# Optimization experiments

Hardware: AMD Instinct MI355X
Metric: run time of the kernel (lower is better)

The kernel has to match this reference:

```python
import jax, jax.numpy as jnp
import numpy as np

N, D, H, E = 4096, 256, 8, 131072
HD = D // H
EPS = 1e-5


def layernorm(x, g, b):
    mu = jnp.mean(x, axis=-1, keepdims=True)
    var = jnp.mean((x - mu) ** 2, axis=-1, keepdims=True)
    return (x - mu) * jax.lax.rsqrt(var + EPS) * g + b


def setup_inputs() -> dict:
    key = jax.random.key(0)
    ks = jax.random.split(key, 20)
    s = 1.0 / np.sqrt(D)
    x = jax.random.normal(ks[0], (N, D), jnp.float32)
    adj = jax.random.uniform(ks[1], (N, N)) < 0.01
    adj_mask = adj | jnp.eye(N, dtype=bool)  # self-loops keep softmax rows finite
    edge_index = jax.random.randint(ks[2], (2, E), 0, N, dtype=jnp.int64)
    edge_attr = jax.random.normal(ks[3], (E, D), jnp.float32)
    p = {
        'wq': jax.random.normal(ks[4], (D, D)) * s, 'bq': jnp.zeros((D,)),
        'wk': jax.random.normal(ks[5], (D, D)) * s, 'bk': jnp.zeros((D,)),
        'wv': jax.random.normal(ks[6], (D, D)) * s, 'bv': jnp.zeros((D,)),
        'wo': jax.random.normal(ks[7], (D, D)) * s, 'bo': jnp.zeros((D,)),
        'we': jax.random.normal(ks[8], (D, H)) * s, 'be': jnp.zeros((H,)),
        'w1': jax.random.normal(ks[9], (D, 4 * D)) * s, 'b1': jnp.zeros((4 * D,)),
        'w2': jax.random.normal(ks[10], (4 * D, D)) * (1.0 / np.sqrt(4 * D)), 'b2': jnp.zeros((D,)),
        'g1': jnp.ones((D,)), 'beta1': jnp.zeros((D,)),
        'g2': jnp.ones((D,)), 'beta2': jnp.zeros((D,)),
    }
    return dict(x=x, adj_mask=adj_mask, edge_index=edge_index, edge_attr=edge_attr, **p)


def reference(x, adj_mask, edge_index, edge_attr, wq, bq, wk, bk, wv, bv, wo, bo,
              we, be, w1, b1, w2, b2, g1, beta1, g2, beta2):
    n = x.shape[0]
    Q = (x @ wq + bq).reshape(n, H, HD)
    K = (x @ wk + bk).reshape(n, H, HD)
    V = (x @ wv + bv).reshape(n, H, HD)
    scores = jnp.einsum('nhd,mhd->nmh', Q, K) / np.sqrt(HD)  # [N,N,H]
    edge_bias = edge_attr @ we + be                          # [E,H]
    scores = scores.at[edge_index[0], edge_index[1]].add(edge_bias)
    s = jnp.transpose(scores, (0, 2, 1))                     # [N,H,N]
    s = jnp.where(adj_mask[:, None, :], s, -jnp.inf)
    attn = jax.nn.softmax(s, axis=-1)                        # dropout eval-mode no-op
    ctx = jnp.einsum('nhm,mhd->nhd', attn, V).reshape(n, D)
    attn_out = ctx @ wo + bo
    x1 = layernorm(x + attn_out, g1, beta1)
    ff = jax.nn.gelu(x1 @ w1 + b1, approximate=False) @ w2 + b2
    return layernorm(x1 + ff, g2, beta2)
```

## Files before the change

kernel.cpp:

```cpp
#include <hip/hip_runtime.h>
#include <math.h>

#define NN   4096
#define DD   256
#define HH   8
#define HD   32
#define DFF  1024
#define QKVW 768
#define AC   128
#define EC   128
#define SCPAD 129
#define QSP  36
#define NPB  2

typedef unsigned short ushort_t;
typedef __attribute__((ext_vector_type(8))) short short8;
typedef __attribute__((ext_vector_type(4))) float f32x4;

__device__ __forceinline__ float bf2f(unsigned short u){
  union { unsigned int i; float f; } v; v.i = ((unsigned int)u) << 16; return v.f;
}
__device__ __forceinline__ unsigned short f2bf(float f){
  union { float f; unsigned int i; } v; v.f = f;
  unsigned int x = v.i;
  return (unsigned short)((x + 0x7FFFu + ((x >> 16) & 1u)) >> 16);
}
__device__ __forceinline__ float ldf(const void* p, size_t i, int isbf){
  return isbf ? bf2f(((const ushort_t*)p)[i]) : ((const float*)p)[i];
}
__device__ __forceinline__ ushort_t ldb16(const void* p, size_t i, int isbf){
  return isbf ? ((const ushort_t*)p)[i] : f2bf(((const float*)p)[i]);
}

__global__ void k_detect(const int* __restrict__ adj32, const int* __restrict__ ei32,
                         const unsigned int* __restrict__ g1w, int* __restrict__ flags,
                         int* __restrict__ counts, int* __restrict__ cursor){
  __shared__ int c0s, c1s;
  int t = threadIdx.x;
  if (t == 0) { c0s = 0; c1s = 0; }
  __syncthreads();
  int c0 = 0, c1 = 0;
  for (int i = t; i < 960; i += 256) if (adj32[(size_t)i * 4097] != 0) c0++;
  for (int i = t; i < 2048; i += 256) if (ei32[2*i + 1] != 0) c1++;
  atomicAdd(&c0s, c0); atomicAdd(&c1s, c1);
  for (int i = t; i < NN; i += 256) { counts[i] = 0; cursor[i] = 0; }
  __syncthreads();
  if (t == 0) {
    flags[0] = (c0s == 960) ? 1 : 0;
    flags[1] = (c1s > 100) ? 1 : 0;
    flags[2] = (g1w[0] == 0x3F803F80u) ? 1 : 0;
  }
}

__global__ __launch_bounds__(256) void k_csr(const void* __restrict__ adj,
                                             const int* __restrict__ flags,
                                             int* __restrict__ alist,
                                             int* __restrict__ acnt){
  __shared__ int cntS;
  __shared__ int actS[AC];
  const int n = blockIdx.x, t = threadIdx.x;
  if (t == 0) cntS = 0;
  __syncthreads();
  if (flags[0]) {
    const uint4* arow = (const uint4*)((const int*)adj + (size_t)n * NN);
    #pragma unroll
    for (int i = 0; i < 4; i++) {
      uint4 v = arow[t + 256 * i];
      int c0 = 4 * (t + 256 * i);
      if (v.x) { int p = atomicAdd(&cntS, 1); if (p < AC) actS[p] = c0; }
      if (v.y) { int p = atomicAdd(&cntS, 1); if (p < AC) actS[p] = c0 + 1; }
      if (v.z) { int p = atomicAdd(&cntS, 1); if (p < AC) actS[p] = c0 + 2; }
      if (v.w) { int p = atomicAdd(&cntS, 1); if (p < AC) actS[p] = c0 + 3; }
    }
  } else {
    const uint4* arow = (const uint4*)((const unsigned char*)adj + (size_t)n * NN);
    uint4 v = arow[t];
    unsigned int wsv[4] = {v.x, v.y, v.z, v.w};
    #pragma unroll
    for (int q = 0; q < 4; q++) {
      unsigned int u = wsv[q];
      int c0 = 16 * t + 4 * q;
      if (u & 0x000000FFu) { int p = atomicAdd(&cntS, 1); if (p < AC) actS[p] = c0; }
      if (u & 0x0000FF00u) { int p = atomicAdd(&cntS, 1); if (p < AC) actS[p] = c0 + 1; }
      if (u & 0x00FF0000u) { int p = atomicAdd(&cntS, 1); if (p < AC) actS[p] = c0 + 2; }
      if (u & 0xFF000000u) { int p = atomicAdd(&cntS, 1); if (p < AC) actS[p] = c0 + 3; }
    }
  }
  __syncthreads();
  int m = cntS; if (m > AC) m = AC;
  if (t == 0) acnt[n] = m;
  for (int j = t; j < m; j += 256) alist[(size_t)n * AC + j] = actS[j];
}

#define NX    (NN * DD)
#define NWE   (DD * HH)
#define TPREP 768
__global__ __launch_bounds__(256) void k_prep(
    const void* __restrict__ x, const void* __restrict__ wq, const void* __restrict__ wk,
    const void* __restrict__ wv, const void* __restrict__ wo, const void* __restrict__ w1,
    const void* __restrict__ w2, const void* __restrict__ we,
    const void* __restrict__ bq, const void* __restrict__ bk, const void* __restrict__ bv,
    const void* __restrict__ bo, const void* __restrict__ be, const void* __restrict__ b1,
    const void* __restrict__ b2, const void* __restrict__ g1, const void* __restrict__ be1,
    const void* __restrict__ g2, const void* __restrict__ be2,
    const int* __restrict__ ei, const int* __restrict__ flags,
    ushort_t* __restrict__ xb,
    ushort_t* __restrict__ wqkvT, ushort_t* __restrict__ woT,
    ushort_t* __restrict__ w1T, ushort_t* __restrict__ w2T,
    float* __restrict__ wef, float* __restrict__ bqkvf,
    float* __restrict__ bof, float* __restrict__ bef,
    float* __restrict__ b1f, float* __restrict__ b2f,
    float* __restrict__ g1f, float* __restrict__ be1f,
    float* __restrict__ g2f, float* __restrict__ be2f,
    int* __restrict__ counts, int E, int TOT)
{
  const int isbf = flags[2];
  const int t = threadIdx.x;
  if (blockIdx.x < TPREP) {
    __shared__ ushort_t tile[32][36];
    int b = blockIdx.x;
    const void* src; ushort_t* dst; int R, C, ti;
    if (b < 64)       { src = wq; dst = wqkvT;              R = 256;  C = 256;  ti = b; }
    else if (b < 128) { src = wk; dst = wqkvT + 256 * 256;  R = 256;  C = 256;  ti = b - 64; }
    else if (b < 192) { src = wv; dst = wqkvT + 512 * 256;  R = 256;  C = 256;  ti = b - 128; }
    else if (b < 256) { src = wo; dst = woT;                R = 256;  C = 256;  ti = b - 192; }
    else if (b < 512) { src = w1; dst = w1T;                R = 256;  C = 1024; ti = b - 256; }
    else              { src = w2; dst = w2T;                R = 1024; C = 256;  ti = b - 512; }
    int tiles_c = C >> 5;
    int tr = ti / tiles_c, tc = ti - tr * tiles_c;
    int lr = t >> 3, lc0 = (t & 7) << 2;
    size_t sbase = (size_t)(tr * 32 + lr) * C + tc * 32 + lc0;
    if (isbf) {
      const ushort_t* s16 = (const ushort_t*)src + sbase;
      tile[lr][lc0+0] = s16[0]; tile[lr][lc0+1] = s16[1];
      tile[lr][lc0+2] = s16[2]; tile[lr][lc0+3] = s16[3];
    } else {
      const float4* sf = (const float4*)((const float*)src + sbase);
      float4 v = *sf;
      tile[lr][lc0+0] = f2bf(v.x); tile[lr][lc0+1] = f2bf(v.y);
      tile[lr][lc0+2] = f2bf(v.z); tile[lr][lc0+3] = f2bf(v.w);
    }
    __syncthreads();
    int i = t >> 3, j0 = (t & 7) << 2;
    ushort_t* dp = dst + (size_t)(tc * 32 + i) * R + tr * 32 + j0;
    ushort_t o0 = tile[j0][i], o1 = tile[j0+1][i], o2 = tile[j0+2][i], o3 = tile[j0+3][i];
    dp[0] = o0; dp[1] = o1; dp[2] = o2; dp[3] = o3;
    return;
  }
  const int ei32 = flags[1];
  const int stride = (gridDim.x - TPREP) * 256;
  for (int i = (blockIdx.x - TPREP) * 256 + t; i < TOT; i += stride) {
    int r = i;
    if (r < NX) { xb[r] = ldb16(x, r, isbf); continue; }
    r -= NX;
    if (r < E) {
      int src = ei32 ? ei[r] : ei[2 * r];
      if ((unsigned)src < (unsigned)NN) atomicAdd(&counts[src], 1);
      continue;
    }
    r -= E;
    if (r < NWE) { wef[r] = ldf(we, r, isbf); continue; }
    r -= NWE;
    if (r < QKVW) {
      const void* bs = (r < 256) ? bq : (r < 512) ? bk : bv;
      bqkvf[r] = ldf(bs, r & 255, isbf);
      continue;
    }
    r -= QKVW;
    if (r < DD)  { bof[r] = ldf(bo, r, isbf); continue; }   r -= DD;
    if (r < HH)  { bef[r] = ldf(be, r, isbf); continue; }   r -= HH;
    if (r < DFF) { b1f[r] = ldf(b1, r, isbf); continue; }   r -= DFF;
    if (r < DD)  { b2f[r] = ldf(b2, r, isbf); continue; }   r -= DD;
    if (r < DD)  { g1f[r] = ldf(g1, r, isbf); continue; }   r -= DD;
    if (r < DD)  { be1f[r] = ldf(be1, r, isbf); continue; } r -= DD;
    if (r < DD)  { g2f[r] = ldf(g2, r, isbf); continue; }   r -= DD;
    if (r < DD)  { be2f[r] = ldf(be2, r, isbf); }
  }
}

#define LDK 72
__global__ __launch_bounds__(256) void k_gemm(
    const ushort_t* __restrict__ A, const ushort_t* __restrict__ Bt,
    const float* __restrict__ bias, void* __restrict__ C,
    int M, int Nn, int K, int act, int mode,
    float* __restrict__ qf, ushort_t* __restrict__ kbuf, ushort_t* __restrict__ vbuf)
{
  __shared__ ushort_t As[64 * LDK];
  __shared__ ushort_t Bs[64 * LDK];
  const int t = threadIdx.x;
  const int wave = t >> 6, lane = t & 63;
  const int l15 = lane & 15, quad = lane >> 4;
  const int wr = wave >> 1, wc = wave & 1;
  const int bm0 = blockIdx.y * 64, bn0 = blockIdx.x * 64;

  const int arow = t >> 2, akg = (t & 3) << 4;

  f32x4 acc[2][2] = {};

  const ushort_t* ap = A  + (size_t)(bm0 + arow) * K + akg;
  const ushort_t* bp = Bt + (size_t)(bn0 + arow) * K + akg;
  uint4 a0 = *(const uint4*)ap;
  uint4 a1 = *(const uint4*)(ap + 8);
  uint4 b0 = *(const uint4*)bp;
  uint4 b1 = *(const uint4*)(bp + 8);

  for (int k0 = 0; k0 < K; k0 += 64) {
    __syncthreads();
    *(uint4*)(&As[arow * LDK + akg]) = a0;
    *(uint4*)(&As[arow * LDK + akg + 8]) = a1;
    *(uint4*)(&Bs[arow * LDK + akg]) = b0;
    *(uint4*)(&Bs[arow * LDK + akg + 8]) = b1;
    __syncthreads();
    if (k0 + 64 < K) {
      a0 = *(const uint4*)(ap + k0 + 64);
      a1 = *(const uint4*)(ap + k0 + 64 + 8);
      b0 = *(const uint4*)(bp + k0 + 64);
      b1 = *(const uint4*)(bp + k0 + 64 + 8);
    }
    #pragma unroll
    for (int kk = 0; kk < 2; kk++) {
      short8 af[2], bf[2];
      #pragma unroll
      for (int fr = 0; fr < 2; fr++)
        af[fr] = *(const short8*)(&As[(wr * 32 + fr * 16 + l15) * LDK + kk * 32 + quad * 8]);
      #pragma unroll
      for (int fc = 0; fc < 2; fc++)
        bf[fc] = *(const short8*)(&Bs[(wc * 32 + fc * 16 + l15) * LDK + kk * 32 + quad * 8]);
      #pragma unroll
      for (int fr = 0; fr < 2; fr++)
        #pragma unroll
        for (int fc = 0; fc < 2; fc++)
          acc[fr][fc] = __builtin_amdgcn_mfma_f32_16x16x32_bf16(af[fr], bf[fc], acc[fr][fc], 0, 0, 0);
    }
  }

  #pragma unroll
  for (int fr = 0; fr < 2; fr++) {
    #pragma unroll
    for (int fc = 0; fc < 2; fc++) {
      int gn = bn0 + wc * 32 + fc * 16 + l15;
      float bcol = bias[gn];
      #pragma unroll
      for (int r = 0; r < 4; r++) {
        int gm = bm0 + wr * 32 + fr * 16 + quad * 4 + r;
        float v = acc[fr][fc][r] + bcol;
        if (act) v = 0.5f * v * (1.0f + erff(v * 0.70710678118654752f));
        if (mode == 2) {
          if (gn < 256)      qf[(size_t)gm * 256 + gn] = v;
          else if (gn < 512) kbuf[(size_t)gm * 256 + (gn - 256)] = f2bf(v);
          else               vbuf[(size_t)gm * 256 + (gn - 512)] = f2bf(v);
        } else {
          ((ushort_t*)C)[(size_t)gm * Nn + gn] = f2bf(v);
        }
      }
    }
  }
}

__global__ __launch_bounds__(512) void k_gemmln(
    const ushort_t* __restrict__ A, const ushort_t* __restrict__ Bt,
    const float* __restrict__ bias, const void* __restrict__ res, int res_raw,
    void* __restrict__ outf, ushort_t* __restrict__ outb,
    const float* __restrict__ g, const float* __restrict__ beta,
    int final_mode, const int* __restrict__ flags, int K)
{
  __shared__ ushort_t As[16 * LDK];
  __shared__ ushort_t Bs[256 * LDK];
  __shared__ float p1[16][8];
  __shared__ float p2[16][8];
  const int t = threadIdx.x;
  const int wave = t >> 6, lane = t & 63;
  const int l15 = lane & 15, quad = lane >> 4;
  const int bm0 = blockIdx.x * 16;

  const int arow = t >> 3, akg = (t & 7) << 3;
  const int brow = t >> 1, bkg = (t & 1) << 5;

  f32x4 acc[2] = {};

  const ushort_t* ap = A + (size_t)(bm0 + arow) * K + akg;
  const ushort_t* bp = Bt + (size_t)brow * K + bkg;
  uint4 a0{};
  if (t < 128) a0 = *(const uint4*)ap;
  uint4 b0 = *(const uint4*)bp;
  uint4 b1 = *(const uint4*)(bp + 8);
  uint4 b2 = *(const uint4*)(bp + 16);
  uint4 b3 = *(const uint4*)(bp + 24);

  for (int k0 = 0; k0 < K; k0 += 64) {
    __syncthreads();
    if (t < 128) *(uint4*)(&As[arow * LDK + akg]) = a0;
    *(uint4*)(&Bs[brow * LDK + bkg])      = b0;
    *(uint4*)(&Bs[brow * LDK + bkg + 8])  = b1;
    *(uint4*)(&Bs[brow * LDK + bkg + 16]) = b2;
    *(uint4*)(&Bs[brow * LDK + bkg + 24]) = b3;
    __syncthreads();
    if (k0 + 64 < K) {
      if (t < 128) a0 = *(const uint4*)(ap + k0 + 64);
      b0 = *(const uint4*)(bp + k0 + 64);
      b1 = *(const uint4*)(bp + k0 + 64 + 8);
      b2 = *(const uint4*)(bp + k0 + 64 + 16);
      b3 = *(const uint4*)(bp + k0 + 64 + 24);
    }
    #pragma unroll
    for (int kk = 0; kk < 2; kk++) {
      short8 af  = *(const short8*)(&As[l15 * LDK + kk * 32 + quad * 8]);
      short8 bf0 = *(const short8*)(&Bs[(wave * 32 +      l15) * LDK + kk * 32 + quad * 8]);
      short8 bf1 = *(const short8*)(&Bs[(wave * 32 + 16 + l15) * LDK + kk * 32 + quad * 8]);
      acc[0] = __builtin_amdgcn_mfma_f32_16x16x32_bf16(af, bf0, acc[0], 0, 0, 0);
      acc[1] = __builtin_amdgcn_mfma_f32_16x16x32_bf16(af, bf1, acc[1], 0, 0, 0);
    }
  }

  const int isbf = flags[2];
  float v[2][4];
  #pragma unroll
  for (int fc = 0; fc < 2; fc++) {
    int gn = wave * 32 + fc * 16 + l15;
    float bc = bias[gn];
    #pragma unroll
    for (int r = 0; r < 4; r++) {
      int gm = bm0 + quad * 4 + r;
      float rv = res_raw ? ldf(res, (size_t)gm * DD + gn, isbf)
                         : ((const float*)res)[(size_t)gm * DD + gn];
      v[fc][r] = acc[fc][r] + bc + rv;
    }
  }
  float s1[4];
  #pragma unroll
  for (int r = 0; r < 4; r++) {
    s1[r] = v[0][r] + v[1][r];
    #pragma unroll
    for (int o = 1; o < 16; o <<= 1) s1[r] += __shfl_xor(s1[r], o, 64);
  }
  if (l15 == 0) {
    #pragma unroll
    for (int r = 0; r < 4; r++) p1[quad * 4 + r][wave] = s1[r];
  }
  __syncthreads();
  float mu[4];
  #pragma unroll
  for (int r = 0; r < 4; r++) {
    float m = 0.f;
    #pragma unroll
    for (int w = 0; w < 8; w++) m += p1[quad * 4 + r][w];
    mu[r] = m * (1.0f / 256.0f);
  }
  float s2[4];
  #pragma unroll
  for (int r = 0; r < 4; r++) {
    float d0 = v[0][r] - mu[r], d1 = v[1][r] - mu[r];
    s2[r] = d0 * d0 + d1 * d1;
    #pragma unroll
    for (int o = 1; o < 16; o <<= 1) s2[r] += __shfl_xor(s2[r], o, 64);
  }
  if (l15 == 0) {
    #pragma unroll
    for (int r = 0; r < 4; r++) p2[quad * 4 + r][wave] = s2[r];
  }
  __syncthreads();
  float rs[4];
  #pragma unroll
  for (int r = 0; r < 4; r++) {
    float q = 0.f;
    #pragma unroll
    for (int w = 0; w < 8; w++) q += p2[quad * 4 + r][w];
    rs[r] = rsqrtf(q * (1.0f / 256.0f) + 1e-5f);
  }
  #pragma unroll
  for (int fc = 0; fc < 2; fc++) {
    int gn = wave * 32 + fc * 16 + l15;
    float gv = g[gn], bv = beta[gn];
    #pragma unroll
    for (int r = 0; r < 4; r++) {
      int gm = bm0 + quad * 4 + r;
      float res_v = (v[fc][r] - mu[r]) * rs[r] * gv + bv;
      if (outb) {
        ((float*)outf)[(size_t)gm * DD + gn] = res_v;
        outb[(size_t)gm * DD + gn] = f2bf(res_v);
      } else {
        if (final_mode && isbf)
          ((ushort_t*)outf)[(size_t)gm * DD + gn] = f2bf(res_v);
        else
          ((float*)outf)[(size_t)gm * DD + gn] = res_v;
      }
    }
  }
}

__global__ __launch_bounds__(256) void k_scan(const int* __restrict__ counts,
                                              int* __restrict__ off){
  __shared__ int wsum[4];
  const int t = threadIdx.x, lid = t & 63, wid = t >> 6;
  int loc[16]; int s = 0;
  #pragma unroll
  for (int j = 0; j < 16; j++) { loc[j] = counts[t * 16 + j]; s += loc[j]; }
  const int tot = s;
  #pragma unroll
  for (int o = 1; o < 64; o <<= 1) {
    int u = __shfl_up(s, o, 64);
    if (lid >= o) s += u;
  }
  if (lid == 63) wsum[wid] = s;
  __syncthreads();
  int pre = 0;
  #pragma unroll
  for (int w = 0; w < 4; w++) if (w < wid) pre += wsum[w];
  int run = pre + s - tot;
  if (t == 0) off[0] = 0;
  #pragma unroll
  for (int j = 0; j < 16; j++) { run += loc[j]; off[t * 16 + j + 1] = run; }
}

__global__ __launch_bounds__(256) void k_ebias(
    const void* __restrict__ ea, const float* __restrict__ wef,
    const float* __restrict__ bef, float* __restrict__ sbias,
    int E, const int* __restrict__ flags,
    const int* __restrict__ ei, const int* __restrict__ off,
    int* __restrict__ cursor, int* __restrict__ sdst, int* __restrict__ seid)
{
  __shared__ float wel[HH * DD];
  int t = threadIdx.x;
  #pragma unroll
  for (int j = 0; j < 8; j++) wel[j * DD + t] = wef[t * 8 + j];
  const int isbf = flags[2];
  if (t < 32) {
    int i = blockIdx.x * 32 + t;
    if (i < E) {
      int src, dst;
      if (flags[1]) { src = ei[i];     dst = ei[E + i]; }
      else          { src = ei[2 * i]; dst = ei[2 * (E + i)]; }
      if ((unsigned)src < (unsigned)NN) {
        if ((unsigned)dst >= (unsigned)NN) dst = 0;
        int pos = off[src] + atomicAdd(&cursor[src], 1);
        sdst[pos] = dst; seid[pos] = i;
      }
    }
  }
  __syncthreads();
  int idx = blockIdx.x * 256 + t;
  int e = idx >> 3, p = idx & 7;
  float acc[8] = {};
  if (e < E) {
    if (isbf) {
      const uint4* base = (const uint4*)((const ushort_t*)ea + (size_t)e * DD);
      #pragma unroll
      for (int q = 0; q < 4; q++) {
        uint4 u = base[q * 8 + p];
        int dbase = 64 * q + 8 * p;
        float f[8];
        union { unsigned int i; float f; } cv;
        cv.i = u.x << 16; f[0] = cv.f; cv.i = u.x & 0xFFFF0000u; f[1] = cv.f;
        cv.i = u.y << 16; f[2] = cv.f; cv.i = u.y & 0xFFFF0000u; f[3] = cv.f;
        cv.i = u.z << 16; f[4] = cv.f; cv.i = u.z & 0xFFFF0000u; f[5] = cv.f;
        cv.i = u.w << 16; f[6] = cv.f; cv.i = u.w & 0xFFFF0000u; f[7] = cv.f;
        #pragma unroll
        for (int j = 0; j < 8; j++)
          #pragma unroll
          for (int h = 0; h < 8; h++)
            acc[h] = fmaf(f[j], wel[h * DD + dbase + j], acc[h]);
      }
    } else {
      const float4* base = (const float4*)((const float*)ea + (size_t)e * DD);
      #pragma unroll
      for (int q = 0; q < 8; q++) {
        float4 u = base[q * 8 + p];
        int dbase = 32 * q + 4 * p;
        #pragma unroll
        for (int h = 0; h < 8; h++) {
          acc[h] = fmaf(u.x, wel[h * DD + dbase + 0], acc[h]);
          acc[h] = fmaf(u.y, wel[h * DD + dbase + 1], acc[h]);
          acc[h] = fmaf(u.z, wel[h * DD + dbase + 2], acc[h]);
          acc[h] = fmaf(u.w, wel[h * DD + dbase + 3], acc[h]);
        }
      }
    }
  }
  #pragma unroll
  for (int h = 0; h < 8; h++) {
    acc[h] += __shfl_xor(acc[h], 1, 8);
    acc[h] += __shfl_xor(acc[h], 2, 8);
    acc[h] += __shfl_xor(acc[h], 4, 8);
  }
  if (e < E) sbias[(size_t)e * 8 + p] = acc[p] + bef[p];
}

__global__ __launch_bounds__(256) void k_attn(
    const float* __restrict__ qf, const ushort_t* __restrict__ kb,
    const ushort_t* __restrict__ vb,
    const int* __restrict__ alist, const int* __restrict__ acnt,
    const int* __restrict__ off, const int* __restrict__ sdst,
    const int* __restrict__ seid, const float* __restrict__ sbias,
    ushort_t* __restrict__ ctxb)
{
  __shared__ float qs[NPB][HH * QSP];
  __shared__ int   act[NPB][AC];
  __shared__ float sc[NPB][HH][SCPAD];
  __shared__ int   edst[NPB][EC];
  __shared__ float ivs[NPB][HH];

  const int t = threadIdx.x;
  const int n0 = blockIdx.x * NPB;

  int na[NPB], cn[NPB], st[NPB];
  #pragma unroll
  for (int s = 0; s < NPB; s++) {
    int n = n0 + s;
    qs[s][(t >> 5) * QSP + (t & 31)] = qf[(size_t)n * DD + t];
    na[s] = min(acnt[n], AC);
    st[s] = off[n];
    int c = off[n + 1] - st[s];
    cn[s] = c < 0 ? 0 : (c > EC ? EC : c);
    for (int j = t; j < na[s]; j += 256) act[s][j] = alist[(size_t)n * AC + j];
    for (int j = t; j < cn[s]; j += 256) edst[s][j] = sdst[st[s] + j];
  }
  __syncthreads();

  #pragma unroll
  for (int s = 0; s < NPB; s++) {
    for (int item = t; item < na[s] * HH; item += 256) {
      int idx = item >> 3, h = item & 7;
      int m = act[s][idx];
      const uint4* kr = (const uint4*)(kb + (size_t)m * DD + h * HD);
      const float* qh = qs[s] + h * QSP;
      float a = 0.f;
      #pragma unroll
      for (int q4 = 0; q4 < 4; q4++) {
        uint4 u = kr[q4];
        int b = q4 * 8;
        union { unsigned int i; float f; } cv;
        cv.i = u.x << 16;         a = fmaf(cv.f, qh[b+0], a);
        cv.i = u.x & 0xFFFF0000u; a = fmaf(cv.f, qh[b+1], a);
        cv.i = u.y << 16;         a = fmaf(cv.f, qh[b+2], a);
        cv.i = u.y & 0xFFFF0000u; a = fmaf(cv.f, qh[b+3], a);
        cv.i = u.z << 16;         a = fmaf(cv.f, qh[b+4], a);
        cv.i = u.z & 0xFFFF0000u; a = fmaf(cv.f, qh[b+5], a);
        cv.i = u.w << 16;         a = fmaf(cv.f, qh[b+6], a);
        cv.i = u.w & 0xFFFF0000u; a = fmaf(cv.f, qh[b+7], a);
      }
      sc[s][h][idx] = a * 0.17677669529663687f;
    }
  }
  __syncthreads();

  #pragma unroll
  for (int s = 0; s < NPB; s++) {
    for (int item = t; item < cn[s] * HH; item += 256) {
      int j = item >> 3, h = item & 7;
      int sid = seid[st[s] + j];
      int dst = edst[s][j];
      int pos = -1;
      for (int i = 0; i < na[s]; i++) if (act[s][i] == dst) { pos = i; break; }
      if (pos >= 0) atomicAdd(&sc[s][h][pos], sbias[(size_t)sid * 8 + h]);
    }
  }
  __syncthreads();

  #pragma unroll
  for (int s = 0; s < NPB; s++) {
    const int h = t >> 5, l = t & 31;
    float lm = -1e30f;
    for (int i = l; i < na[s]; i += 32) lm = fmaxf(lm, sc[s][h][i]);
    #pragma unroll
    for (int o = 16; o > 0; o >>= 1) lm = fmaxf(lm, __shfl_down(lm, o, 32));
    lm = __shfl(lm, 0, 32);
    float ls = 0.f;
    for (int i = l; i < na[s]; i += 32) {
      float e = __expf(sc[s][h][i] - lm);
      sc[s][h][i] = e;
      ls += e;
    }
    #pragma unroll
    for (int o = 16; o > 0; o >>= 1) ls += __shfl_down(ls, o, 32);
    if (l == 0) ivs[s][h] = 1.0f / ls;
  }
  __syncthreads();

  {
    const int s_ = t >> 7, h = (t >> 4) & 7, dp = t & 15;
    const int n_a = s_ ? na[1] : na[0];
    const ushort_t* vcol = vb + h * HD + 2 * dp;
    const float* scp = sc[s_][h];
    float a0 = 0.f, a1 = 0.f;
    int i = 0;
    for (; i + 8 <= n_a; i += 8) {
      int mm[8]; unsigned int vv[8];
      #pragma unroll
      for (int u = 0; u < 8; u++) mm[u] = act[s_][i + u];
      #pragma unroll
      for (int u = 0; u < 8; u++) vv[u] = *(const unsigned int*)(vcol + (size_t)mm[u] * DD);
      #pragma unroll
      for (int u = 0; u < 8; u++) {
        float p = scp[i + u];
        a0 = fmaf(p, bf2f((ushort_t)(vv[u] & 0xFFFFu)), a0);
        a1 = fmaf(p, bf2f((ushort_t)(vv[u] >> 16)), a1);
      }
    }
    for (; i < n_a; i++) {
      unsigned int v = *(const unsigned int*)(vcol + (size_t)act[s_][i] * DD);
      float p = scp[i];
      a0 = fmaf(p, bf2f((ushort_t)(v & 0xFFFFu)), a0);
      a1 = fmaf(p, bf2f((ushort_t)(v >> 16)), a1);
    }
    float iv = ivs[s_][h];
    unsigned int ob = ((unsigned int)f2bf(a1 * iv) << 16) | (unsigned int)f2bf(a0 * iv);
    *(unsigned int*)(ctxb + (size_t)(n0 + s_) * DD + h * HD + 2 * dp) = ob;
  }
}

extern "C" void kernel_launch(void* const* d_in, const int* in_sizes, int n_in,
                              void* d_out, int out_size, void* d_ws, size_t ws_size,
                              hipStream_t stream)
{
  const void* x   = d_in[0];
  const void* adj = d_in[1];
  const int*  ei  = (const int*)d_in[2];
  const void* ea  = d_in[3];
  const void* wq  = d_in[4];  const void* bq  = d_in[5];
  const void* wk  = d_in[6];  const void* bk  = d_in[7];
  const void* wv  = d_in[8];  const void* bv  = d_in[9];
  const void* wo  = d_in[10]; const void* bo  = d_in[11];
  const void* we  = d_in[12]; const void* be  = d_in[13];
  const void* w1  = d_in[14]; const void* b1  = d_in[15];
  const void* w2  = d_in[16]; const void* b2  = d_in[17];
  const void* g1  = d_in[18]; const void* be1 = d_in[19];
  const void* g2  = d_in[20]; const void* be2 = d_in[21];
  const int E = in_sizes[2] / 2;

  char* w = (char*)d_ws;
  size_t o = 0;
  auto carve = [&](size_t bytes) -> void* {
    void* p = w + o; o = (o + bytes + 255) & ~(size_t)255; return p;
  };
  ushort_t* xb    = (ushort_t*)carve((size_t)NN * DD * 2);
  float*    qfb   = (float*)   carve((size_t)NN * DD * 4);
  ushort_t* kbuf  = (ushort_t*)carve((size_t)NN * DD * 2);
  ushort_t* vbuf  = (ushort_t*)carve((size_t)NN * DD * 2);
  ushort_t* wqkvT = (ushort_t*)carve((size_t)QKVW * DD * 2);
  float*    bqkvf = (float*)   carve(QKVW * 4);
  ushort_t* woT   = (ushort_t*)carve((size_t)DD * DD * 2);
  ushort_t* w1T   = (ushort_t*)carve((size_t)DFF * DD * 2);
  ushort_t* w2T   = (ushort_t*)carve((size_t)DD * DFF * 2);
  float*    wef   = (float*)   carve((size_t)DD * HH * 4);
  float*    bof   = (float*)   carve(DD * 4);
  float*    bef   = (float*)   carve(HH * 4);
  float*    b1f   = (float*)   carve(DFF * 4);
  float*    b2f   = (float*)   carve(DD * 4);
  float*    g1f   = (float*)   carve(DD * 4);
  float*    be1f  = (float*)   carve(DD * 4);
  float*    g2f   = (float*)   carve(DD * 4);
  float*    be2f  = (float*)   carve(DD * 4);
  int*      counts = (int*)carve((size_t)NN * 4);
  int*      cursor = (int*)carve((size_t)NN * 4);
  int*      off    = (int*)carve((size_t)(NN + 1) * 4);
  int*      sdst   = (int*)carve((size_t)E * 4);
  int*      seid   = (int*)carve((size_t)E * 4);
  float*    sbias  = (float*)carve((size_t)E * HH * 4);
  int*      alist  = (int*)carve((size_t)NN * AC * 4);
  int*      acnt   = (int*)carve((size_t)NN * 4);
  ushort_t* ctxb     = (ushort_t*)carve((size_t)NN * DD * 2);
  float*    x1f      = (float*)   carve((size_t)NN * DD * 4);
  ushort_t* x1b      = (ushort_t*)carve((size_t)NN * DD * 2);
  ushort_t* hbufb    = (ushort_t*)carve((size_t)NN * DFF * 2);
  int*      flags    = (int*)carve(4 * 4);

  k_detect<<<1, 256, 0, stream>>>((const int*)adj, ei, (const unsigned int*)g1,
                                  flags, counts, cursor);
  k_csr<<<NN, 256, 0, stream>>>(adj, flags, alist, acnt);

  const int TOT = NX + E + NWE + QKVW + DD + HH + DFF + DD + DD + DD + DD + DD;
  k_prep<<<TPREP + 1280, 256, 0, stream>>>(
      x, wq, wk, wv, wo, w1, w2, we, bq, bk, bv, bo, be, b1, b2,
      g1, be1, g2, be2, ei, flags,
      xb, wqkvT, woT, w1T, w2T, wef, bqkvf,
      bof, bef, b1f, b2f, g1f, be1f, g2f, be2f, counts, E, TOT);

  k_scan<<<1, 256, 0, stream>>>(counts, off);
  k_ebias<<<(E * 8 + 255) / 256, 256, 0, stream>>>(ea, wef, bef, sbias, E, flags,
                                                   ei, off, cursor, sdst, seid);

  k_gemm<<<dim3(QKVW / 64, NN / 64), 256, 0, stream>>>(
      xb, wqkvT, bqkvf, nullptr, NN, QKVW, DD, 0, 2, qfb, kbuf, vbuf);

  k_attn<<<NN / NPB, 256, 0, stream>>>(qfb, kbuf, vbuf, alist, acnt, off, sdst,
                                       seid, sbias, ctxb);

  k_gemmln<<<NN / 16, 512, 0, stream>>>(
      ctxb, woT, bof, x, 1, x1f, x1b, g1f, be1f, 0, flags, DD);

  k_gemm<<<dim3(DFF / 64, NN / 64), 256, 0, stream>>>(
      x1b, w1T, b1f, hbufb, NN, DFF, DD, 1, 1, nullptr, nullptr, nullptr);

  k_gemmln<<<NN / 16, 512, 0, stream>>>(
      hbufb, w2T, b2f, x1f, 0, d_out, nullptr, g2f, be2f, 1, flags, DFF);
}
```

Before: 410.1 us.

## Merge CSR build into prep kernel and fuse QKV GEMM with edge-bias kernel

The adjacency-to-list CSR kernel now runs as extra blocks of the prep kernel, and the QKV projection GEMM and edge-bias/edge-scatter kernel now share one launch, split by block index. This cuts two kernel launches and lets independent work overlap on the GPU instead of running back to back. The cost is a larger shared-memory footprint per block in the merged kernels, which may lower occupancy, and the QKV GEMM body is now a duplicated copy.

```diff
diff --git a/kernel.cpp b/kernel.cpp
--- a/kernel.cpp
+++ b/kernel.cpp
@@ -52,50 +52,12 @@
   }
 }
 
-__global__ __launch_bounds__(256) void k_csr(const void* __restrict__ adj,
-                                             const int* __restrict__ flags,
-                                             int* __restrict__ alist,
-                                             int* __restrict__ acnt){
-  __shared__ int cntS;
-  __shared__ int actS[AC];
-  const int n = blockIdx.x, t = threadIdx.x;
-  if (t == 0) cntS = 0;
-  __syncthreads();
-  if (flags[0]) {
-    const uint4* arow = (const uint4*)((const int*)adj + (size_t)n * NN);
-    #pragma unroll
-    for (int i = 0; i < 4; i++) {
-      uint4 v = arow[t + 256 * i];
-      int c0 = 4 * (t + 256 * i);
-      if (v.x) { int p = atomicAdd(&cntS, 1); if (p < AC) actS[p] = c0; }
-      if (v.y) { int p = atomicAdd(&cntS, 1); if (p < AC) actS[p] = c0 + 1; }
-      if (v.z) { int p = atomicAdd(&cntS, 1); if (p < AC) actS[p] = c0 + 2; }
-      if (v.w) { int p = atomicAdd(&cntS, 1); if (p < AC) actS[p] = c0 + 3; }
-    }
-  } else {
-    const uint4* arow = (const uint4*)((const unsigned char*)adj + (size_t)n * NN);
-    uint4 v = arow[t];
-    unsigned int wsv[4] = {v.x, v.y, v.z, v.w};
-    #pragma unroll
-    for (int q = 0; q < 4; q++) {
-      unsigned int u = wsv[q];
-      int c0 = 16 * t + 4 * q;
-      if (u & 0x000000FFu) { int p = atomicAdd(&cntS, 1); if (p < AC) actS[p] = c0; }
-      if (u & 0x0000FF00u) { int p = atomicAdd(&cntS, 1); if (p < AC) actS[p] = c0 + 1; }
-      if (u & 0x00FF0000u) { int p = atomicAdd(&cntS, 1); if (p < AC) actS[p] = c0 + 2; }
-      if (u & 0xFF000000u) { int p = atomicAdd(&cntS, 1); if (p < AC) actS[p] = c0 + 3; }
-    }
-  }
-  __syncthreads();
-  int m = cntS; if (m > AC) m = AC;
-  if (t == 0) acnt[n] = m;
-  for (int j = t; j < m; j += 256) alist[(size_t)n * AC + j] = actS[j];
-}
-
 #define NX    (NN * DD)
 #define NWE   (DD * HH)
 #define TPREP 768
+#define NCSR  NN
 __global__ __launch_bounds__(256) void k_prep(
+    const void* __restrict__ adj, int* __restrict__ alist, int* __restrict__ acnt,
     const void* __restrict__ x, const void* __restrict__ wq, const void* __restrict__ wk,
     const void* __restrict__ wv, const void* __restrict__ wo, const void* __restrict__ w1,
     const void* __restrict__ w2, const void* __restrict__ we,
@@ -116,9 +78,46 @@
 {
   const int isbf = flags[2];
   const int t = threadIdx.x;
-  if (blockIdx.x < TPREP) {
+  if (blockIdx.x < NCSR) {
+    __shared__ int cntS;
+    __shared__ int actS[AC];
+    const int n = blockIdx.x;
+    if (t == 0) cntS = 0;
+    __syncthreads();
+    if (flags[0]) {
+      const uint4* arow = (const uint4*)((const int*)adj + (size_t)n * NN);
+      #pragma unroll
+      for (int i = 0; i < 4; i++) {
+        uint4 v = arow[t + 256 * i];
+        int c0 = 4 * (t + 256 * i);
+        if (v.x) { int p = atomicAdd(&cntS, 1); if (p < AC) actS[p] = c0; }
+        if (v.y) { int p = atomicAdd(&cntS, 1); if (p < AC) actS[p] = c0 + 1; }
+        if (v.z) { int p = atomicAdd(&cntS, 1); if (p < AC) actS[p] = c0 + 2; }
+        if (v.w) { int p = atomicAdd(&cntS, 1); if (p < AC) actS[p] = c0 + 3; }
+      }
+    } else {
+      const uint4* arow = (const uint4*)((const unsigned char*)adj + (size_t)n * NN);
+      uint4 v = arow[t];
+      unsigned int wsv[4] = {v.x, v.y, v.z, v.w};
+      #pragma unroll
+      for (int q = 0; q < 4; q++) {
+        unsigned int u = wsv[q];
+        int c0 = 16 * t + 4 * q;
+        if (u & 0x000000FFu) { int p = atomicAdd(&cntS, 1); if (p < AC) actS[p] = c0; }
+        if (u & 0x0000FF00u) { int p = atomicAdd(&cntS, 1); if (p < AC) actS[p] = c0 + 1; }
+        if (u & 0x00FF0000u) { int p = atomicAdd(&cntS, 1); if (p < AC) actS[p] = c0 + 2; }
+        if (u & 0xFF000000u) { int p = atomicAdd(&cntS, 1); if (p < AC) actS[p] = c0 + 3; }
+      }
+    }
+    __syncthreads();
+    int m = cntS; if (m > AC) m = AC;
+    if (t == 0) acnt[n] = m;
+    for (int j = t; j < m; j += 256) alist[(size_t)n * AC + j] = actS[j];
+    return;
+  }
+  if (blockIdx.x < NCSR + TPREP) {
     __shared__ ushort_t tile[32][36];
-    int b = blockIdx.x;
+    int b = blockIdx.x - NCSR;
     const void* src; ushort_t* dst; int R, C, ti;
     if (b < 64)       { src = wq; dst = wqkvT;              R = 256;  C = 256;  ti = b; }
     else if (b < 128) { src = wk; dst = wqkvT + 256 * 256;  R = 256;  C = 256;  ti = b - 64; }
@@ -148,8 +147,8 @@
     return;
   }
   const int ei32 = flags[1];
-  const int stride = (gridDim.x - TPREP) * 256;
-  for (int i = (blockIdx.x - TPREP) * 256 + t; i < TOT; i += stride) {
+  const int stride = (gridDim.x - NCSR - TPREP) * 256;
+  for (int i = (blockIdx.x - NCSR - TPREP) * 256 + t; i < TOT; i += stride) {
     int r = i;
     if (r < NX) { xb[r] = ldb16(x, r, isbf); continue; }
     r -= NX;
@@ -255,6 +254,151 @@
       }
     }
   }
+}
+
+__global__ __launch_bounds__(256) void k_mid(
+    const ushort_t* __restrict__ A, const ushort_t* __restrict__ Bt,
+    const float* __restrict__ bias,
+    float* __restrict__ qf, ushort_t* __restrict__ kbuf, ushort_t* __restrict__ vbuf,
+    const void* __restrict__ ea, const float* __restrict__ wef,
+    const float* __restrict__ bef, float* __restrict__ sbias,
+    int E, const int* __restrict__ flags,
+    const int* __restrict__ ei, const int* __restrict__ off,
+    int* __restrict__ cursor, int* __restrict__ sdst, int* __restrict__ seid)
+{
+  __shared__ __align__(16) char smem[64 * LDK * 2 * 2];
+  const int t = threadIdx.x;
+  if (blockIdx.x < 768) {
+    ushort_t* As = (ushort_t*)smem;
+    ushort_t* Bs = As + 64 * LDK;
+    const int wave = t >> 6, lane = t & 63;
+    const int l15 = lane & 15, quad = lane >> 4;
+    const int wr = wave >> 1, wc = wave & 1;
+    const int bn0 = (blockIdx.x % 12) * 64, bm0 = (blockIdx.x / 12) * 64;
+    const int arow = t >> 2, akg = (t & 3) << 4;
+    const int K = DD;
+
+    f32x4 acc[2][2] = {};
+
+    const ushort_t* ap = A  + (size_t)(bm0 + arow) * K + akg;
+    const ushort_t* bp = Bt + (size_t)(bn0 + arow) * K + akg;
+    uint4 a0 = *(const uint4*)ap;
+    uint4 a1 = *(const uint4*)(ap + 8);
+    uint4 b0 = *(const uint4*)bp;
+    uint4 b1 = *(const uint4*)(bp + 8);
+
+    for (int k0 = 0; k0 < K; k0 += 64) {
+      __syncthreads();
+      *(uint4*)(&As[arow * LDK + akg]) = a0;
+      *(uint4*)(&As[arow * LDK + akg + 8]) = a1;
+      *(uint4*)(&Bs[arow * LDK + akg]) = b0;
+      *(uint4*)(&Bs[arow * LDK + akg + 8]) = b1;
+      __syncthreads();
+      if (k0 + 64 < K) {
+        a0 = *(const uint4*)(ap + k0 + 64);
+        a1 = *(const uint4*)(ap + k0 + 64 + 8);
+        b0 = *(const uint4*)(bp + k0 + 64);
+        b1 = *(const uint4*)(bp + k0 + 64 + 8);
+      }
+      #pragma unroll
+      for (int kk = 0; kk < 2; kk++) {
+        short8 af[2], bf[2];
+        #pragma unroll
+        for (int fr = 0; fr < 2; fr++)
+          af[fr] = *(const short8*)(&As[(wr * 32 + fr * 16 + l15) * LDK + kk * 32 + quad * 8]);
+        #pragma unroll
+        for (int fc = 0; fc < 2; fc++)
+          bf[fc] = *(const short8*)(&Bs[(wc * 32 + fc * 16 + l15) * LDK + kk * 32 + quad * 8]);
+        #pragma unroll
+        for (int fr = 0; fr < 2; fr++)
+          #pragma unroll
+          for (int fc = 0; fc < 2; fc++)
+            acc[fr][fc] = __builtin_amdgcn_mfma_f32_16x16x32_bf16(af[fr], bf[fc], acc[fr][fc], 0, 0, 0);
+      }
+    }
+
+    #pragma unroll
+    for (int fr = 0; fr < 2; fr++) {
+      #pragma unroll
+      for (int fc = 0; fc < 2; fc++) {
+        int gn = bn0 + wc * 32 + fc * 16 + l15;
+        float bcol = bias[gn];
+        #pragma unroll
+        for (int r = 0; r < 4; r++) {
+          int gm = bm0 + wr * 32 + fr * 16 + quad * 4 + r;
+          float v = acc[fr][fc][r] + bcol;
+          if (gn < 256)      qf[(size_t)gm * 256 + gn] = v;
+          else if (gn < 512) kbuf[(size_t)gm * 256 + (gn - 256)] = f2bf(v);
+          else               vbuf[(size_t)gm * 256 + (gn - 512)] = f2bf(v);
+        }
+      }
+    }
+    return;
+  }
+  float* wel = (float*)smem;
+  const int b = blockIdx.x - 768;
+  #pragma unroll
+  for (int j = 0; j < 8; j++) wel[j * DD + t] = wef[t * 8 + j];
+  const int isbf = flags[2];
+  if (t < 32) {
+    int i = b * 32 + t;
+    if (i < E) {
+      int src, dst;
+      if (flags[1]) { src = ei[i];     dst = ei[E + i]; }
+      else          { src = ei[2 * i]; dst = ei[2 * (E + i)]; }
+      if ((unsigned)src < (unsigned)NN) {
+        if ((unsigned)dst >= (unsigned)NN) dst = 0;
+        int pos = off[src] + atomicAdd(&cursor[src], 1);
+        sdst[pos] = dst; seid[pos] = i;
+      }
+    }
+  }
+  __syncthreads();
+  int idx = b * 256 + t;
+  int e = idx >> 3, p = idx & 7;
+  float acc[8] = {};
+  if (e < E) {
+    if (isbf) {
+      const uint4* base = (const uint4*)((const ushort_t*)ea + (size_t)e * DD);
+      #pragma unroll
+      for (int q = 0; q < 4; q++) {
+        uint4 u = base[q * 8 + p];
+        int dbase = 64 * q + 8 * p;
+        float f[8];
+        union { unsigned int i; float f; } cv;
+        cv.i = u.x << 16; f[0] = cv.f; cv.i = u.x & 0xFFFF0000u; f[1] = cv.f;
+        cv.i = u.y << 16; f[2] = cv.f; cv.i = u.y & 0xFFFF0000u; f[3] = cv.f;
+        cv.i = u.z << 16; f[4] = cv.f; cv.i = u.z & 0xFFFF0000u; f[5] = cv.f;
+        cv.i = u.w << 16; f[6] = cv.f; cv.i = u.w & 0xFFFF0000u; f[7] = cv.f;
+        #pragma unroll
+        for (int j = 0; j < 8; j++)
+          #pragma unroll
+          for (int h = 0; h < 8; h++)
+            acc[h] = fmaf(f[j], wel[h * DD + dbase + j], acc[h]);
+      }
+    } else {
+      const float4* base = (const float4*)((const float*)ea + (size_t)e * DD);
+      #pragma unroll
+      for (int q = 0; q < 8; q++) {
+        float4 u = base[q * 8 + p];
+        int dbase = 32 * q + 4 * p;
+        #pragma unroll
+        for (int h = 0; h < 8; h++) {
+          acc[h] = fmaf(u.x, wel[h * DD + dbase + 0], acc[h]);
+          acc[h] = fmaf(u.y, wel[h * DD + dbase + 1], acc[h]);
+          acc[h] = fmaf(u.z, wel[h * DD + dbase + 2], acc[h]);
+          acc[h] = fmaf(u.w, wel[h * DD + dbase + 3], acc[h]);
+        }
+      }
+    }
+  }
+  #pragma unroll
+  for (int h = 0; h < 8; h++) {
+    acc[h] += __shfl_xor(acc[h], 1, 8);
+    acc[h] += __shfl_xor(acc[h], 2, 8);
+    acc[h] += __shfl_xor(acc[h], 4, 8);
+  }
+  if (e < E) sbias[(size_t)e * 8 + p] = acc[p] + bef[p];
 }
 
 __global__ __launch_bounds__(512) void k_gemmln(
@@ -410,79 +554,6 @@
   if (t == 0) off[0] = 0;
   #pragma unroll
   for (int j = 0; j < 16; j++) { run += loc[j]; off[t * 16 + j + 1] = run; }
-}
-
-__global__ __launch_bounds__(256) void k_ebias(
-    const void* __restrict__ ea, const float* __restrict__ wef,
-    const float* __restrict__ bef, float* __restrict__ sbias,
-    int E, const int* __restrict__ flags,
-    const int* __restrict__ ei, const int* __restrict__ off,
-    int* __restrict__ cursor, int* __restrict__ sdst, int* __restrict__ seid)
-{
-  __shared__ float wel[HH * DD];
-  int t = threadIdx.x;
-  #pragma unroll
-  for (int j = 0; j < 8; j++) wel[j * DD + t] = wef[t * 8 + j];
-  const int isbf = flags[2];
-  if (t < 32) {
-    int i = blockIdx.x * 32 + t;
-    if (i < E) {
-      int src, dst;
-      if (flags[1]) { src = ei[i];     dst = ei[E + i]; }
-      else          { src = ei[2 * i]; dst = ei[2 * (E + i)]; }
-      if ((unsigned)src < (unsigned)NN) {
-        if ((unsigned)dst >= (unsigned)NN) dst = 0;
-        int pos = off[src] + atomicAdd(&cursor[src], 1);
-        sdst[pos] = dst; seid[pos] = i;
-      }
-    }
-  }
-  __syncthreads();
-  int idx = blockIdx.x * 256 + t;
-  int e = idx >> 3, p = idx & 7;
-  float acc[8] = {};
-  if (e < E) {
-    if (isbf) {
-      const uint4* base = (const uint4*)((const ushort_t*)ea + (size_t)e * DD);
-      #pragma unroll
-      for (int q = 0; q < 4; q++) {
-        uint4 u = base[q * 8 + p];
-        int dbase = 64 * q + 8 * p;
-        float f[8];
-        union { unsigned int i; float f; } cv;
-        cv.i = u.x << 16; f[0] = cv.f; cv.i = u.x & 0xFFFF0000u; f[1] = cv.f;
-        cv.i = u.y << 16; f[2] = cv.f; cv.i = u.y & 0xFFFF0000u; f[3] = cv.f;
-        cv.i = u.z << 16; f[4] = cv.f; cv.i = u.z & 0xFFFF0000u; f[5] = cv.f;
-        cv.i = u.w << 16; f[6] = cv.f; cv.i = u.w & 0xFFFF0000u; f[7] = cv.f;
-        #pragma unroll
-        for (int j = 0; j < 8; j++)
-          #pragma unroll
-          for (int h = 0; h < 8; h++)
-            acc[h] = fmaf(f[j], wel[h * DD + dbase + j], acc[h]);
-      }
-    } else {
-      const float4* base = (const float4*)((const float*)ea + (size_t)e * DD);
-      #pragma unroll
-      for (int q = 0; q < 8; q++) {
-        float4 u = base[q * 8 + p];
-        int dbase = 32 * q + 4 * p;
-        #pragma unroll
-        for (int h = 0; h < 8; h++) {
-          acc[h] = fmaf(u.x, wel[h * DD + dbase + 0], acc[h]);
-          acc[h] = fmaf(u.y, wel[h * DD + dbase + 1], acc[h]);
-          acc[h] = fmaf(u.z, wel[h * DD + dbase + 2], acc[h]);
-          acc[h] = fmaf(u.w, wel[h * DD + dbase + 3], acc[h]);
-        }
-      }
-    }
-  }
-  #pragma unroll
-  for (int h = 0; h < 8; h++) {
-    acc[h] += __shfl_xor(acc[h], 1, 8);
-    acc[h] += __shfl_xor(acc[h], 2, 8);
-    acc[h] += __shfl_xor(acc[h], 4, 8);
-  }
-  if (e < E) sbias[(size_t)e * 8 + p] = acc[p] + bef[p];
 }
 
 __global__ __launch_bounds__(256) void k_attn(
@@ -666,21 +737,21 @@
 
   k_detect<<<1, 256, 0, stream>>>((const int*)adj, ei, (const unsigned int*)g1,
                                   flags, counts, cursor);
-  k_csr<<<NN, 256, 0, stream>>>(adj, flags, alist, acnt);
 
   const int TOT = NX + E + NWE + QKVW + DD + HH + DFF + DD + DD + DD + DD + DD;
-  k_prep<<<TPREP + 1280, 256, 0, stream>>>(
+  k_prep<<<NCSR + TPREP + 1280, 256, 0, stream>>>(
+      adj, alist, acnt,
       x, wq, wk, wv, wo, w1, w2, we, bq, bk, bv, bo, be, b1, b2,
       g1, be1, g2, be2, ei, flags,
       xb, wqkvT, woT, w1T, w2T, wef, bqkvf,
       bof, bef, b1f, b2f, g1f, be1f, g2f, be2f, counts, E, TOT);
 
   k_scan<<<1, 256, 0, stream>>>(counts, off);
-  k_ebias<<<(E * 8 + 255) / 256, 256, 0, stream>>>(ea, wef, bef, sbias, E, flags,
-                                                   ei, off, cursor, sdst, seid);
-
-  k_gemm<<<dim3(QKVW / 64, NN / 64), 256, 0, stream>>>(
-      xb, wqkvT, bqkvf, nullptr, NN, QKVW, DD, 0, 2, qfb, kbuf, vbuf);
+
+  int ebb = (E * 8 + 255) / 256;
+  k_mid<<<768 + ebb, 256, 0, stream>>>(
+      xb, wqkvT, bqkvf, qfb, kbuf, vbuf,
+      ea, wef, bef, sbias, E, flags, ei, off, cursor, sdst, seid);
 
   k_attn<<<NN / NPB, 256, 0, stream>>>(qfb, kbuf, vbuf, alist, acnt, off, sdst,
                                        seid, sbias, ctxb);
```

Result: faster. 400.3 us (-2.4%).
